# Kernel tuning notes

Measured on AMD Instinct MI355X. Metric: run time of the kernel, lower is better.

## Reference

```python
import jax, jax.numpy as jnp
import numpy as np

L = 16          # quantization levels (MSB LUT)
UP = 2          # upscale factor
H, W = 2048, 2048

# neighbor offsets (x, y) for pixels b and c per kernel type: 'h', 'd', 'b'
_OFFSETS = [((0, 1), (0, 2)),   # h: horizontal
            ((1, 1), (2, 2)),   # d: diagonal
            ((1, 2), (2, 1))]   # b: anti-diagonal-ish


def setup_inputs() -> dict:
    key = jax.random.key(0)
    k1, k2 = jax.random.split(key)
    img_lr = jax.random.randint(k1, (H, W), 0, L, dtype=jnp.int32)
    msb_weight = jax.random.normal(k2, (3, L ** 3, UP * UP), dtype=jnp.float32)
    return {"img_lr": img_lr, "msb_weight": msb_weight}


def reference(img_lr, msb_weight):
    up = UP
    out = jnp.zeros((img_lr.shape[0] * up, img_lr.shape[1] * up), jnp.float32)
    for k in range(3):  # kernel types h, d, b
        (xb, yb), (xc, yc) = _OFFSETS[k]
        w = msb_weight[k]                         # [L^3, up*up]
        for r in range(4):                        # 4-fold rotation ensemble
            rot = jnp.rot90(img_lr, r)            # get_slice rotation
            dx, dy = rot.shape
            p = jnp.pad(rot, ((0, 2), (0, 2)), mode='reflect')
            a = p[:dx, :dy]                       # anchor pixel (0,0)
            b = p[xb:xb + dx, yb:yb + dy]
            c = p[xc:xc + dx, yc:yc + dy]
            idx = (a * (L * L) + b * L + c).reshape(-1)  # composite LUT index
            # gather, then interleave the up x up sub-pixels spatially
            tmp = w[idx].reshape(dx, dy, up, up)
            tmp = tmp.transpose(0, 2, 1, 3).reshape(dx * up, dy * up)
            out = out + jnp.rot90(tmp, (4 - r) % 4)      # rotate back
    return out / 3.0
```

## Files before the change

### kernel.cpp

```cpp
#include <hip/hip_runtime.h>
#include <hip/hip_fp16.h>

#define N 2048
#define ONW 4096
#define TW 128
#define TH 32
#define HW 132
#define HH 36
#define HELEMS (HW * HH)
#define LUT_ENTRIES 12288
#define LUT_BYTES (LUT_ENTRIES * 8)
#define SMEM_BYTES (LUT_BYTES + 2 * HELEMS * 4)

typedef _Float16 half4v __attribute__((ext_vector_type(4)));
typedef float fvec4 __attribute__((ext_vector_type(4)));

__device__ __forceinline__ int reflect(int i) {
    i = i < 0 ? -i : i;
    return i >= N ? 2 * N - 2 - i : i;
}

__global__ __launch_bounds__(1024, 4) void hdblut_kernel(
    const int* __restrict__ img, const float4* __restrict__ w4,
    float* __restrict__ out)
{
    extern __shared__ unsigned char smem[];
    half4v* lut = (half4v*)smem;
    int* bufs = (int*)(smem + LUT_BYTES);

    const int tx = threadIdx.x;
    const int ty = threadIdx.y;
    const int tid = ty * 64 + tx;
    const int x0 = (int)(blockIdx.x & 15) * TW;
    const int y0 = (int)(blockIdx.x >> 4) * (TH * 4);

    #pragma unroll
    for (int i = 0; i < 12; ++i) {
        int j = tid + i * 1024;
        float4 v = w4[j];
        half4v h;
        h.x = (_Float16)v.x; h.y = (_Float16)v.y;
        h.z = (_Float16)v.z; h.w = (_Float16)v.w;
        lut[j] = h;
    }

    for (int e = tid; e < HELEMS; e += 1024) {
        int rr = e / HW, cc = e - rr * HW;
        bufs[e] = img[reflect(y0 + rr - 2) * N + reflect(x0 + cc - 2)];
    }
    __syncthreads();

    const int bo[3][2] = {{0, 1}, {1, 1}, {1, 2}};
    const int co[3][2] = {{0, 2}, {2, 2}, {2, 1}};
    const float s = 1.0f / 3.0f;
    fvec4* o4 = (fvec4*)out;

    int pre[5];
    #pragma unroll 1
    for (int t = 0; t < 4; ++t) {
        int* cur = bufs + (t & 1) * HELEMS;
        int* nxt = bufs + ((t + 1) & 1) * HELEMS;

        if (t < 3) {
            const int yb = y0 + (t + 1) * TH;
            #pragma unroll
            for (int u = 0; u < 5; ++u) {
                int e = tid + u * 1024;
                if (e < HELEMS) {
                    int rr = e / HW, cc = e - rr * HW;
                    pre[u] = img[reflect(yb + rr - 2) * N + reflect(x0 + cc - 2)];
                }
            }
        }

        int n[6][6];
        {
            const int r0 = 2 * ty, c0 = 2 * tx;
            #pragma unroll
            for (int r = 0; r < 6; ++r)
                #pragma unroll
                for (int j = 0; j < 3; ++j) {
                    int2 t2 = *(const int2*)&cur[(r0 + r) * HW + c0 + 2 * j];
                    n[r][2 * j] = t2.x; n[r][2 * j + 1] = t2.y;
                }
        }

        float acc[2][2][4];
        #pragma unroll
        for (int i = 0; i < 2; ++i)
            #pragma unroll
            for (int j = 0; j < 2; ++j)
                #pragma unroll
                for (int c = 0; c < 4; ++c) acc[i][j][c] = 0.f;

        #pragma unroll
        for (int pi = 0; pi < 2; ++pi) {
          #pragma unroll
          for (int pj = 0; pj < 2; ++pj) {
            const int abase = n[2 + pi][2 + pj] << 8;

            int idx[12];
            #pragma unroll
            for (int r = 0; r < 4; ++r) {
              #pragma unroll
              for (int k = 0; k < 3; ++k) {
                const int bp = bo[k][0], bq = bo[k][1];
                const int cp = co[k][0], cq = co[k][1];
                const int bdi = (r == 0) ? bp : (r == 1) ? bq : (r == 2) ? -bp : -bq;
                const int bdj = (r == 0) ? bq : (r == 1) ? -bp : (r == 2) ? -bq : bp;
                const int cdi = (r == 0) ? cp : (r == 1) ? cq : (r == 2) ? -cp : -cq;
                const int cdj = (r == 0) ? cq : (r == 1) ? -cp : (r == 2) ? -cq : cp;
                const int bv = n[pi + 2 + bdi][pj + 2 + bdj];
                const int cv = n[pi + 2 + cdi][pj + 2 + cdj];
                idx[r * 3 + k] = (k << 12) | abase | (bv << 4) | cv;
              }
            }

            half4v v[12];
            #pragma unroll
            for (int i = 0; i < 12; ++i) v[i] = lut[idx[i]];

            float* o = acc[pi][pj];
            #pragma unroll
            for (int r = 0; r < 4; ++r) {
                half4v S = v[3 * r] + v[3 * r + 1] + v[3 * r + 2];
                const float x = (float)S.x, y = (float)S.y;
                const float z = (float)S.z, w = (float)S.w;
                if (r == 0)      { o[0] += x; o[1] += y; o[2] += z; o[3] += w; }
                else if (r == 1) { o[0] += z; o[1] += x; o[2] += w; o[3] += y; }
                else if (r == 2) { o[0] += w; o[1] += z; o[2] += y; o[3] += x; }
                else             { o[0] += y; o[1] += w; o[2] += x; o[3] += z; }
            }
          }
        }

        const int py = y0 + t * TH + 2 * ty;
        const int ox = (x0 + 2 * tx) * 2;
        {
            fvec4 v0 = {acc[0][0][0] * s, acc[0][0][1] * s, acc[0][1][0] * s, acc[0][1][1] * s};
            fvec4 v1 = {acc[0][0][2] * s, acc[0][0][3] * s, acc[0][1][2] * s, acc[0][1][3] * s};
            fvec4 v2 = {acc[1][0][0] * s, acc[1][0][1] * s, acc[1][1][0] * s, acc[1][1][1] * s};
            fvec4 v3 = {acc[1][0][2] * s, acc[1][0][3] * s, acc[1][1][2] * s, acc[1][1][3] * s};
            o4[((2 * py + 0) * ONW + ox) >> 2] = v0;
            o4[((2 * py + 1) * ONW + ox) >> 2] = v1;
            o4[((2 * py + 2) * ONW + ox) >> 2] = v2;
            o4[((2 * py + 3) * ONW + ox) >> 2] = v3;
        }

        if (t < 3) {
            #pragma unroll
            for (int u = 0; u < 5; ++u) {
                int e = tid + u * 1024;
                if (e < HELEMS) nxt[e] = pre[u];
            }
        }
        __syncthreads();
    }
}

extern "C" void kernel_launch(void* const* d_in, const int* in_sizes, int n_in,
                              void* d_out, int out_size, void* d_ws, size_t ws_size,
                              hipStream_t stream)
{
    const int* img = (const int*)d_in[0];
    const float4* w4 = (const float4*)d_in[1];
    float* out = (float*)d_out;
    (void)hipFuncSetAttribute(reinterpret_cast<const void*>(hdblut_kernel),
                              hipFuncAttributeMaxDynamicSharedMemorySize, SMEM_BYTES);
    hdblut_kernel<<<dim3(256), dim3(64, 16), SMEM_BYTES, stream>>>(img, w4, out);
}
```

Baseline: 98.22 us.

## Read image neighborhoods directly from global memory instead of LDS double-buffer

Removes the LDS halo tile and its double-buffered prefetch; each thread now loads its 6x6 neighborhood straight from global memory (vector int2 loads on interior columns, reflected scalar loads at the edges). This drops the per-iteration __syncthreads and the LDS traffic for image data, leaving LDS for the LUT only. It also pre-shifts neighbor values and batches 24 LUT gathers per row pair to expose more memory-level parallelism. The cost is redundant global and L2 reads of overlapping neighborhoods across threads, and no explicit prefetch to hide load latency.

```diff
diff --git a/kernel.cpp b/kernel.cpp
--- a/kernel.cpp
+++ b/kernel.cpp
@@ -3,14 +3,8 @@
 
 #define N 2048
 #define ONW 4096
-#define TW 128
-#define TH 32
-#define HW 132
-#define HH 36
-#define HELEMS (HW * HH)
 #define LUT_ENTRIES 12288
-#define LUT_BYTES (LUT_ENTRIES * 8)
-#define SMEM_BYTES (LUT_BYTES + 2 * HELEMS * 4)
+#define SMEM_BYTES (LUT_ENTRIES * 8)
 
 typedef _Float16 half4v __attribute__((ext_vector_type(4)));
 typedef float fvec4 __attribute__((ext_vector_type(4)));
@@ -26,13 +20,12 @@
 {
     extern __shared__ unsigned char smem[];
     half4v* lut = (half4v*)smem;
-    int* bufs = (int*)(smem + LUT_BYTES);
 
     const int tx = threadIdx.x;
     const int ty = threadIdx.y;
     const int tid = ty * 64 + tx;
-    const int x0 = (int)(blockIdx.x & 15) * TW;
-    const int y0 = (int)(blockIdx.x >> 4) * (TH * 4);
+    const int x0 = (int)(blockIdx.x & 15) * 128;
+    const int y0 = (int)(blockIdx.x >> 4) * 128;
 
     #pragma unroll
     for (int i = 0; i < 12; ++i) {
@@ -43,11 +36,6 @@
         h.z = (_Float16)v.z; h.w = (_Float16)v.w;
         lut[j] = h;
     }
-
-    for (int e = tid; e < HELEMS; e += 1024) {
-        int rr = e / HW, cc = e - rr * HW;
-        bufs[e] = img[reflect(y0 + rr - 2) * N + reflect(x0 + cc - 2)];
-    }
     __syncthreads();
 
     const int bo[3][2] = {{0, 1}, {1, 1}, {1, 2}};
@@ -55,34 +43,31 @@
     const float s = 1.0f / 3.0f;
     fvec4* o4 = (fvec4*)out;
 
-    int pre[5];
+    const int gj0 = x0 + 2 * tx - 2;
+    const bool fastx = (gj0 >= 0) && (gj0 + 5 < N);
+
     #pragma unroll 1
     for (int t = 0; t < 4; ++t) {
-        int* cur = bufs + (t & 1) * HELEMS;
-        int* nxt = bufs + ((t + 1) & 1) * HELEMS;
+        const int py0 = y0 + t * 32 + 2 * ty;
 
-        if (t < 3) {
-            const int yb = y0 + (t + 1) * TH;
+        int n[6][6], m[6][6];
+        #pragma unroll
+        for (int r = 0; r < 6; ++r) {
+            const int rb = reflect(py0 - 2 + r) * N;
+            if (fastx) {
+                int2 a = *(const int2*)&img[rb + gj0];
+                int2 b = *(const int2*)&img[rb + gj0 + 2];
+                int2 c = *(const int2*)&img[rb + gj0 + 4];
+                n[r][0] = a.x; n[r][1] = a.y;
+                n[r][2] = b.x; n[r][3] = b.y;
+                n[r][4] = c.x; n[r][5] = c.y;
+            } else {
+                #pragma unroll
+                for (int c = 0; c < 6; ++c)
+                    n[r][c] = img[rb + reflect(gj0 + c)];
+            }
             #pragma unroll
-            for (int u = 0; u < 5; ++u) {
-                int e = tid + u * 1024;
-                if (e < HELEMS) {
-                    int rr = e / HW, cc = e - rr * HW;
-                    pre[u] = img[reflect(yb + rr - 2) * N + reflect(x0 + cc - 2)];
-                }
-            }
-        }
-
-        int n[6][6];
-        {
-            const int r0 = 2 * ty, c0 = 2 * tx;
-            #pragma unroll
-            for (int r = 0; r < 6; ++r)
-                #pragma unroll
-                for (int j = 0; j < 3; ++j) {
-                    int2 t2 = *(const int2*)&cur[(r0 + r) * HW + c0 + 2 * j];
-                    n[r][2 * j] = t2.x; n[r][2 * j + 1] = t2.y;
-                }
+            for (int c = 0; c < 6; ++c) m[r][c] = n[r][c] << 4;
         }
 
         float acc[2][2][4];
@@ -95,66 +80,56 @@
 
         #pragma unroll
         for (int pi = 0; pi < 2; ++pi) {
-          #pragma unroll
-          for (int pj = 0; pj < 2; ++pj) {
-            const int abase = n[2 + pi][2 + pj] << 8;
+            int idx[24];
+            #pragma unroll
+            for (int pj = 0; pj < 2; ++pj) {
+                const int abase = n[2 + pi][2 + pj] << 8;
+                #pragma unroll
+                for (int r = 0; r < 4; ++r) {
+                    #pragma unroll
+                    for (int k = 0; k < 3; ++k) {
+                        const int bp = bo[k][0], bq = bo[k][1];
+                        const int cp = co[k][0], cq = co[k][1];
+                        const int bdi = (r == 0) ? bp : (r == 1) ? bq : (r == 2) ? -bp : -bq;
+                        const int bdj = (r == 0) ? bq : (r == 1) ? -bp : (r == 2) ? -bq : bp;
+                        const int cdi = (r == 0) ? cp : (r == 1) ? cq : (r == 2) ? -cp : -cq;
+                        const int cdj = (r == 0) ? cq : (r == 1) ? -cp : (r == 2) ? -cq : cp;
+                        idx[pj * 12 + r * 3 + k] =
+                            ((k << 12) + abase) + m[pi + 2 + bdi][pj + 2 + bdj]
+                                                + n[pi + 2 + cdi][pj + 2 + cdj];
+                    }
+                }
+            }
+            half4v v[24];
+            #pragma unroll
+            for (int i = 0; i < 24; ++i) v[i] = lut[idx[i]];
 
-            int idx[12];
             #pragma unroll
-            for (int r = 0; r < 4; ++r) {
-              #pragma unroll
-              for (int k = 0; k < 3; ++k) {
-                const int bp = bo[k][0], bq = bo[k][1];
-                const int cp = co[k][0], cq = co[k][1];
-                const int bdi = (r == 0) ? bp : (r == 1) ? bq : (r == 2) ? -bp : -bq;
-                const int bdj = (r == 0) ? bq : (r == 1) ? -bp : (r == 2) ? -bq : bp;
-                const int cdi = (r == 0) ? cp : (r == 1) ? cq : (r == 2) ? -cp : -cq;
-                const int cdj = (r == 0) ? cq : (r == 1) ? -cp : (r == 2) ? -cq : cp;
-                const int bv = n[pi + 2 + bdi][pj + 2 + bdj];
-                const int cv = n[pi + 2 + cdi][pj + 2 + cdj];
-                idx[r * 3 + k] = (k << 12) | abase | (bv << 4) | cv;
-              }
+            for (int pj = 0; pj < 2; ++pj) {
+                float* o = acc[pi][pj];
+                #pragma unroll
+                for (int r = 0; r < 4; ++r) {
+                    half4v S = v[pj * 12 + 3 * r] + v[pj * 12 + 3 * r + 1]
+                                                  + v[pj * 12 + 3 * r + 2];
+                    const float x = (float)S.x, y = (float)S.y;
+                    const float z = (float)S.z, w = (float)S.w;
+                    if (r == 0)      { o[0] += x; o[1] += y; o[2] += z; o[3] += w; }
+                    else if (r == 1) { o[0] += z; o[1] += x; o[2] += w; o[3] += y; }
+                    else if (r == 2) { o[0] += w; o[1] += z; o[2] += y; o[3] += x; }
+                    else             { o[0] += y; o[1] += w; o[2] += x; o[3] += z; }
+                }
             }
-
-            half4v v[12];
-            #pragma unroll
-            for (int i = 0; i < 12; ++i) v[i] = lut[idx[i]];
-
-            float* o = acc[pi][pj];
-            #pragma unroll
-            for (int r = 0; r < 4; ++r) {
-                half4v S = v[3 * r] + v[3 * r + 1] + v[3 * r + 2];
-                const float x = (float)S.x, y = (float)S.y;
-                const float z = (float)S.z, w = (float)S.w;
-                if (r == 0)      { o[0] += x; o[1] += y; o[2] += z; o[3] += w; }
-                else if (r == 1) { o[0] += z; o[1] += x; o[2] += w; o[3] += y; }
-                else if (r == 2) { o[0] += w; o[1] += z; o[2] += y; o[3] += x; }
-                else             { o[0] += y; o[1] += w; o[2] += x; o[3] += z; }
-            }
-          }
         }
 
-        const int py = y0 + t * TH + 2 * ty;
         const int ox = (x0 + 2 * tx) * 2;
-        {
-            fvec4 v0 = {acc[0][0][0] * s, acc[0][0][1] * s, acc[0][1][0] * s, acc[0][1][1] * s};
-            fvec4 v1 = {acc[0][0][2] * s, acc[0][0][3] * s, acc[0][1][2] * s, acc[0][1][3] * s};
-            fvec4 v2 = {acc[1][0][0] * s, acc[1][0][1] * s, acc[1][1][0] * s, acc[1][1][1] * s};
-            fvec4 v3 = {acc[1][0][2] * s, acc[1][0][3] * s, acc[1][1][2] * s, acc[1][1][3] * s};
-            o4[((2 * py + 0) * ONW + ox) >> 2] = v0;
-            o4[((2 * py + 1) * ONW + ox) >> 2] = v1;
-            o4[((2 * py + 2) * ONW + ox) >> 2] = v2;
-            o4[((2 * py + 3) * ONW + ox) >> 2] = v3;
-        }
-
-        if (t < 3) {
-            #pragma unroll
-            for (int u = 0; u < 5; ++u) {
-                int e = tid + u * 1024;
-                if (e < HELEMS) nxt[e] = pre[u];
-            }
-        }
-        __syncthreads();
+        fvec4 v0 = {acc[0][0][0] * s, acc[0][0][1] * s, acc[0][1][0] * s, acc[0][1][1] * s};
+        fvec4 v1 = {acc[0][0][2] * s, acc[0][0][3] * s, acc[0][1][2] * s, acc[0][1][3] * s};
+        fvec4 v2 = {acc[1][0][0] * s, acc[1][0][1] * s, acc[1][1][0] * s, acc[1][1][1] * s};
+        fvec4 v3 = {acc[1][0][2] * s, acc[1][0][3] * s, acc[1][1][2] * s, acc[1][1][3] * s};
+        o4[((2 * py0 + 0) * ONW + ox) >> 2] = v0;
+        o4[((2 * py0 + 1) * ONW + ox) >> 2] = v1;
+        o4[((2 * py0 + 2) * ONW + ox) >> 2] = v2;
+        o4[((2 * py0 + 3) * ONW + ox) >> 2] = v3;
     }
 }
 
```

Measured after the change: 105.2 us. +7.1%, slower.
